# Performance work log

Measured on AMD Instinct MI355X. Metric: run time of the kernel, lower is better.

## Reference

```python
import jax, jax.numpy as jnp
import numpy as np

D_IN = 1024
D_OUT = 1024


def setup_inputs() -> dict:
    key = jax.random.key(0)
    kx, kq, kk, kv = jax.random.split(key, 4)
    x = jax.random.normal(kx, (4, 2048, D_IN), dtype=jnp.float32)
    s = 1.0 / np.sqrt(D_IN)
    Wq = jax.random.normal(kq, (D_IN, D_OUT), dtype=jnp.float32) * s
    Wk = jax.random.normal(kk, (D_IN, D_OUT), dtype=jnp.float32) * s
    Wv = jax.random.normal(kv, (D_IN, D_OUT), dtype=jnp.float32) * s
    return {"x": x, "Wq": Wq, "Wk": Wk, "Wv": Wv}


def reference(x, Wq, Wk, Wv):
    # x: [B, S, d_in]; W*: [d_in, d_out]
    B, S, _ = x.shape
    q = x @ Wq  # [B, S, d_out]
    k = x @ Wk
    v = x @ Wv
    scale = 1.0 / jnp.sqrt(jnp.asarray(k.shape[-1], x.dtype))
    scores = jnp.einsum("bqd,bkd->bqk", q, k) * scale  # [B, S, S]
    # causal mask: positions j > i masked to -inf (triu, diagonal=1)
    causal = jnp.tril(jnp.ones((S, S), dtype=bool))
    scores = jnp.where(causal[None, :, :], scores, -jnp.inf)
    attn = jax.nn.softmax(scores, axis=-1)  # dropout p=0.0 -> identity
    return jnp.einsum("bqk,bkd->bqd", attn, v)
```

## Files before the change

kernel.cpp:

```cpp
#include <hip/hip_runtime.h>
#include <hip/hip_bf16.h>

#define NB 4
#define SB 2048
#define DD 1024
#define BM 128
#define BN 128
#define BK 32

typedef __attribute__((ext_vector_type(8))) short bf16x8;
typedef __attribute__((ext_vector_type(4))) short bf16x4;
typedef __attribute__((ext_vector_type(4))) float f32x4;
typedef unsigned int u32;

__device__ __forceinline__ float bf2f(unsigned short u) {
    return __uint_as_float(((u32)u) << 16);
}
__device__ __forceinline__ short f2bf(float f) {
    u32 u = __float_as_uint(f);
    u32 r = (u + 0x7fffu + ((u >> 16) & 1u)) >> 16;
    return (short)r;
}

__device__ __forceinline__ void mfma_step(const short* As, const short* Bs,
                                          f32x4 (&acc)[4][4], int lane, int wave)
{
    const int wm = (wave >> 1) * 64, wn = (wave & 1) * 64;
    const int fr = lane & 15;
    const int quad = lane >> 4;
    bf16x8 af[4], bf[4];
#pragma unroll
    for (int t = 0; t < 4; t++) {
        af[t] = *(const bf16x8*)&As[(wm + t * 16 + fr) * BK + quad * 8];
        bf[t] = *(const bf16x8*)&Bs[(wn + t * 16 + fr) * BK + quad * 8];
    }
#pragma unroll
    for (int mt = 0; mt < 4; mt++)
#pragma unroll
        for (int nt = 0; nt < 4; nt++)
            acc[mt][nt] = __builtin_amdgcn_mfma_f32_16x16x32_bf16(
                af[mt], bf[nt], acc[mt][nt], 0, 0, 0);
}

__device__ __forceinline__ void stage128x32(const short* __restrict__ g, int ld,
                                            short* lds, int tid) {
    const int wave = tid >> 6, lane = tid & 63;
    const int r = lane >> 2;
    const int c = (lane & 3) * 8;
#pragma unroll
    for (int i = 0; i < 2; i++) {
        const int chunk = wave * 2 + i;
        const short* gp = g + (size_t)(chunk * 16 + r) * ld + c;
        __builtin_amdgcn_global_load_lds(
            (const __attribute__((address_space(1))) u32*)gp,
            (__attribute__((address_space(3))) u32*)(lds + chunk * 512 + lane * 8),
            16, 0, 0);
    }
}

__device__ __forceinline__ void stage_f32_128x32(const float* __restrict__ g,
                                                 int ld, short* lds, int tid) {
    const int r = tid >> 1;
    const int c = (tid & 1) * 16;
    const float* gp = &g[(size_t)r * ld + c];
    float4 v0 = *(const float4*)(gp + 0);
    float4 v1 = *(const float4*)(gp + 4);
    float4 v2 = *(const float4*)(gp + 8);
    float4 v3 = *(const float4*)(gp + 12);
    bf16x8 o0, o1;
    o0[0] = f2bf(v0.x); o0[1] = f2bf(v0.y); o0[2] = f2bf(v0.z); o0[3] = f2bf(v0.w);
    o0[4] = f2bf(v1.x); o0[5] = f2bf(v1.y); o0[6] = f2bf(v1.z); o0[7] = f2bf(v1.w);
    o1[0] = f2bf(v2.x); o1[1] = f2bf(v2.y); o1[2] = f2bf(v2.z); o1[3] = f2bf(v2.w);
    o1[4] = f2bf(v3.x); o1[5] = f2bf(v3.y); o1[6] = f2bf(v3.z); o1[7] = f2bf(v3.w);
    *(bf16x8*)&lds[r * BK + c] = o0;
    *(bf16x8*)&lds[r * BK + c + 8] = o1;
}

__device__ __forceinline__ void gemm_bt_body(
    const short* __restrict__ A, int lda, const short* __restrict__ Bt, int ldb,
    int m0, int n0, int kend, short* As, short* Bs, f32x4 (&acc)[4][4], int tid)
{
    const int lane = tid & 63;
    const int wave = tid >> 6;
    for (int k0 = 0; k0 < kend; k0 += BK) {
        stage128x32(A + (size_t)m0 * lda + k0, lda, As, tid);
        stage128x32(Bt + (size_t)n0 * ldb + k0, ldb, Bs, tid);
        __syncthreads();
        mfma_step(As, Bs, acc, lane, wave);
        __syncthreads();
    }
}

__global__ __launch_bounds__(256) void prep_mm(
    const float* __restrict__ x, const float* __restrict__ Wq,
    const float* __restrict__ Wk, const float* __restrict__ Wv,
    short* __restrict__ xb, short* __restrict__ Wvt, float* __restrict__ Mp4)
{
    __shared__ short As[BM * BK], Bs[BN * BK];
    __shared__ short t[64][65];
    const int bx = blockIdx.x;
    const int tid = threadIdx.x;
    if (bx < 256) {
        const int ch = bx >> 6;
        const int t64 = bx & 63;
        const int m0 = (t64 >> 3) * BM;
        const int n0 = (t64 & 7) * BN;
        const int kbase = ch * 256;
        const int lane = tid & 63, wave = tid >> 6;
        f32x4 acc[4][4];
#pragma unroll
        for (int a = 0; a < 4; a++)
#pragma unroll
            for (int b = 0; b < 4; b++) acc[a][b] = (f32x4){0.f, 0.f, 0.f, 0.f};
        for (int k0 = 0; k0 < 256; k0 += BK) {
            stage_f32_128x32(Wk + (size_t)m0 * DD + kbase + k0, DD, As, tid);
            stage_f32_128x32(Wq + (size_t)n0 * DD + kbase + k0, DD, Bs, tid);
            __syncthreads();
            mfma_step(As, Bs, acc, lane, wave);
            __syncthreads();
        }
        const int wm = (wave >> 1) * 64, wn = (wave & 1) * 64;
        const int fr = lane & 15, quad = lane >> 4;
        float* Mc = Mp4 + (size_t)ch * DD * DD;
#pragma unroll
        for (int mt = 0; mt < 4; mt++)
#pragma unroll
            for (int nt = 0; nt < 4; nt++)
#pragma unroll
                for (int r = 0; r < 4; r++) {
                    const size_t m = m0 + wm + mt * 16 + quad * 4 + r;
                    const size_t n = n0 + wn + nt * 16 + fr;
                    Mc[m * DD + n] = acc[mt][nt][r];
                }
        return;
    }
    if (bx < 4352) {
        const size_t i = ((size_t)(bx - 256) * 256 + tid) * 8;
        float4 a = *(const float4*)&x[i];
        float4 b = *(const float4*)&x[i + 4];
        bf16x8 o;
        o[0] = f2bf(a.x); o[1] = f2bf(a.y); o[2] = f2bf(a.z); o[3] = f2bf(a.w);
        o[4] = f2bf(b.x); o[5] = f2bf(b.y); o[6] = f2bf(b.z); o[7] = f2bf(b.w);
        *(bf16x8*)&xb[i] = o;
        return;
    }
    const int rr = bx - 4352;
    const int k0 = (rr & 15) * 64;
    const int n0 = (rr >> 4) * 64;
    {
        const int r = tid >> 4;
        const int c = (tid & 15) * 4;
#pragma unroll
        for (int i = 0; i < 4; i++) {
            float4 v = *(const float4*)&Wv[(size_t)(k0 + i * 16 + r) * DD + n0 + c];
            t[i * 16 + r][c + 0] = f2bf(v.x);
            t[i * 16 + r][c + 1] = f2bf(v.y);
            t[i * 16 + r][c + 2] = f2bf(v.z);
            t[i * 16 + r][c + 3] = f2bf(v.w);
        }
    }
    __syncthreads();
    {
        const int r = tid >> 3;
        const int c = (tid & 7) * 8;
#pragma unroll
        for (int i = 0; i < 2; i++) {
            bf16x8 o;
#pragma unroll
            for (int j = 0; j < 8; j++) o[j] = t[c + j][i * 32 + r];
            *(bf16x8*)&Wvt[(size_t)(n0 + i * 32 + r) * DD + k0 + c] = o;
        }
    }
}

__global__ __launch_bounds__(256) void mm_reduce(const float* __restrict__ Mp4,
                                                 short* __restrict__ Mp)
{
    const size_t e = ((size_t)blockIdx.x * 256 + threadIdx.x) * 4;
    const size_t N = (size_t)DD * DD;
    float4 s = *(const float4*)&Mp4[e];
#pragma unroll
    for (int c = 1; c < 4; c++) {
        float4 p = *(const float4*)&Mp4[c * N + e];
        s.x += p.x; s.y += p.y; s.z += p.z; s.w += p.w;
    }
    bf16x4 o;
    o[0] = f2bf(s.x); o[1] = f2bf(s.y); o[2] = f2bf(s.z); o[3] = f2bf(s.w);
    *(bf16x4*)&Mp[e] = o;
}

__global__ __launch_bounds__(256) void t_gemm(
    const short* __restrict__ xb, const short* __restrict__ Mp,
    short* __restrict__ T)
{
    __shared__ short As[BM * BK], Bs[BN * BK];
    const int n0 = blockIdx.x * BN;
    const int m0 = blockIdx.y * BM;
    f32x4 acc[4][4];
#pragma unroll
    for (int a = 0; a < 4; a++)
#pragma unroll
        for (int b = 0; b < 4; b++) acc[a][b] = (f32x4){0.f, 0.f, 0.f, 0.f};
    gemm_bt_body(xb, DD, Mp, DD, m0, n0, DD, As, Bs, acc, threadIdx.x);
    const int lane = threadIdx.x & 63, wave = threadIdx.x >> 6;
    const int wm = (wave >> 1) * 64, wn = (wave & 1) * 64;
    const int fr = lane & 15, quad = lane >> 4;
#pragma unroll
    for (int mt = 0; mt < 4; mt++)
#pragma unroll
        for (int nt = 0; nt < 4; nt++)
#pragma unroll
            for (int r = 0; r < 4; r++) {
                const size_t m = m0 + wm + mt * 16 + quad * 4 + r;
                const size_t n = n0 + wn + nt * 16 + fr;
                T[m * DD + n] = f2bf(acc[mt][nt][r]);
            }
}

__global__ __launch_bounds__(256) void v_gemm(
    const short* __restrict__ xb, const short* __restrict__ Wvt,
    short* __restrict__ Vt)
{
    __shared__ short As[BM * BK], Bs[BN * BK];
    const int n0 = blockIdx.x * BN;
    const int m0 = blockIdx.y * BM;
    f32x4 acc[4][4];
#pragma unroll
    for (int a = 0; a < 4; a++)
#pragma unroll
        for (int b = 0; b < 4; b++) acc[a][b] = (f32x4){0.f, 0.f, 0.f, 0.f};
    gemm_bt_body(xb, DD, Wvt, DD, m0, n0, DD, As, Bs, acc, threadIdx.x);
    const int lane = threadIdx.x & 63, wave = threadIdx.x >> 6;
    const int wm = (wave >> 1) * 64, wn = (wave & 1) * 64;
    const int fr = lane & 15, quad = lane >> 4;
    const int bb = m0 >> 11;
    const int s0 = (m0 & (SB - 1)) + wm + quad * 4;
    short* Vb = Vt + (size_t)bb * DD * SB;
#pragma unroll
    for (int mt = 0; mt < 4; mt++)
#pragma unroll
        for (int nt = 0; nt < 4; nt++) {
            const size_t n = n0 + wn + nt * 16 + fr;
            const size_t s = s0 + mt * 16;
            bf16x4 o;
#pragma unroll
            for (int r = 0; r < 4; r++) o[r] = f2bf(acc[mt][nt][r]);
            *(bf16x4*)&Vb[n * SB + s] = o;
        }
}

__global__ __launch_bounds__(256) void scores_mfma(
    const short* __restrict__ T, const short* __restrict__ xb,
    short* __restrict__ Sc)
{
    const int idx = blockIdx.x;
    int qt = (int)((__fsqrt_rn(8.f * idx + 1.f) - 1.f) * 0.5f);
    while ((qt + 1) * (qt + 2) / 2 <= idx) qt++;
    while (qt * (qt + 1) / 2 > idx) qt--;
    const int kt = idx - qt * (qt + 1) / 2;
    const int qm0 = qt * BM;
    const int kn0 = kt * BN;
    const int b = blockIdx.y;
    __shared__ short As[BM * BK], Bs[BN * BK];
    const short* Tb = T + (size_t)b * SB * DD;
    const short* Xb = xb + (size_t)b * SB * DD;
    short* Sb = Sc + (size_t)b * SB * SB;
    f32x4 acc[4][4];
#pragma unroll
    for (int a = 0; a < 4; a++)
#pragma unroll
        for (int c = 0; c < 4; c++) acc[a][c] = (f32x4){0.f, 0.f, 0.f, 0.f};
    gemm_bt_body(Tb, DD, Xb, DD, qm0, kn0, DD, As, Bs, acc, threadIdx.x);
    const int lane = threadIdx.x & 63, wave = threadIdx.x >> 6;
    const int wm = (wave >> 1) * 64, wn = (wave & 1) * 64;
    const int fr = lane & 15, quad = lane >> 4;
    const float scale = 0.03125f;
#pragma unroll
    for (int mt = 0; mt < 4; mt++)
#pragma unroll
        for (int nt = 0; nt < 4; nt++)
#pragma unroll
            for (int r = 0; r < 4; r++) {
                const size_t q = qm0 + wm + mt * 16 + quad * 4 + r;
                const size_t k = kn0 + wn + nt * 16 + fr;
                Sb[q * SB + k] = f2bf(acc[mt][nt][r] * scale);
            }
}

__global__ __launch_bounds__(256) void softmax_kernel(short* __restrict__ Sc)
{
    const int row = blockIdx.x;
    const int i = row & (SB - 1);
    const int jlim = ((i >> 7) + 1) << 7;
    short* r = Sc + (size_t)row * SB;
    const int t = threadIdx.x;
    const int lane = t & 63, wave = t >> 6;
    __shared__ float red[8];

    float v[8];
    float mx = -1e30f;
#pragma unroll
    for (int c = 0; c < 8; c++) {
        const int j = c * 256 + t;
        const float s = (j <= i) ? bf2f((unsigned short)r[j]) : -1e30f;
        v[c] = s;
        mx = fmaxf(mx, s);
    }
#pragma unroll
    for (int o = 32; o > 0; o >>= 1) mx = fmaxf(mx, __shfl_down(mx, o));
    if (lane == 0) red[wave] = mx;
    __syncthreads();
    mx = fmaxf(fmaxf(red[0], red[1]), fmaxf(red[2], red[3]));

    float sum = 0.f;
#pragma unroll
    for (int c = 0; c < 8; c++) {
        const int j = c * 256 + t;
        const float e = (j <= i) ? __expf(v[c] - mx) : 0.f;
        v[c] = e;
        sum += e;
    }
#pragma unroll
    for (int o = 32; o > 0; o >>= 1) sum += __shfl_down(sum, o);
    if (lane == 0) red[4 + wave] = sum;
    __syncthreads();
    const float inv = 1.0f / (red[4] + red[5] + red[6] + red[7]);
#pragma unroll
    for (int c = 0; c < 8; c++) {
        const int j = c * 256 + t;
        if (j < jlim) r[j] = f2bf(v[c] * inv);
    }
}

__global__ __launch_bounds__(256) void pv_mfma(
    const short* __restrict__ P, const short* __restrict__ Vt,
    float* __restrict__ O, float* __restrict__ Pp)
{
    __shared__ short As[BM * BK], Bs[BN * BK];
    const int n0 = blockIdx.x * BN;
    const int y = blockIdx.y;
    const int chunk1 = (y >= 16);
    const int qt = chunk1 ? (y - 8) : y;
    const int qm0 = qt * BM;
    const int kstart = chunk1 ? 1024 : 0;
    const int kstop = chunk1 ? (qt + 1) * BM : min(1024, (qt + 1) * BM);
    const int b = blockIdx.z;
    const short* Pb = P + (size_t)b * SB * SB + kstart;
    const short* Vb = Vt + (size_t)b * DD * SB + kstart;
    f32x4 acc[4][4];
#pragma unroll
    for (int a = 0; a < 4; a++)
#pragma unroll
        for (int c = 0; c < 4; c++) acc[a][c] = (f32x4){0.f, 0.f, 0.f, 0.f};
    gemm_bt_body(Pb, SB, Vb, SB, qm0, n0, kstop - kstart, As, Bs, acc,
                 threadIdx.x);
    const int lane = threadIdx.x & 63, wave = threadIdx.x >> 6;
    const int wm = (wave >> 1) * 64, wn = (wave & 1) * 64;
    const int fr = lane & 15, quad = lane >> 4;
    float* dst = chunk1 ? (Pp + (size_t)b * 1024 * DD)
                        : (O + (size_t)b * SB * DD);
    const int qoff = chunk1 ? 1024 : 0;
#pragma unroll
    for (int mt = 0; mt < 4; mt++)
#pragma unroll
        for (int nt = 0; nt < 4; nt++)
#pragma unroll
            for (int r = 0; r < 4; r++) {
                const size_t q = qm0 + wm + mt * 16 + quad * 4 + r - qoff;
                const size_t n = n0 + wn + nt * 16 + fr;
                dst[q * DD + n] = acc[mt][nt][r];
            }
}

__global__ __launch_bounds__(256) void reduce_pv(const float* __restrict__ Pp,
                                                 float* __restrict__ O)
{
    const size_t e = ((size_t)blockIdx.x * 256 + threadIdx.x) * 4;
    const size_t b = e / ((size_t)1024 * DD);
    const size_t rem = e - b * (size_t)1024 * DD;
    float4 p = *(const float4*)&Pp[e];
    float* o = &O[b * (size_t)SB * DD + (size_t)1024 * DD + rem];
    float4 v = *(const float4*)o;
    v.x += p.x; v.y += p.y; v.z += p.z; v.w += p.w;
    *(float4*)o = v;
}

extern "C" void kernel_launch(void* const* d_in, const int* in_sizes, int n_in,
                              void* d_out, int out_size, void* d_ws, size_t ws_size,
                              hipStream_t stream)
{
    const float* x  = (const float*)d_in[0];
    const float* Wq = (const float*)d_in[1];
    const float* Wk = (const float*)d_in[2];
    const float* Wv = (const float*)d_in[3];
    float* out = (float*)d_out;

    const size_t XE = (size_t)NB * SB * DD;
    const size_t WE = (size_t)DD * DD;
    short* xb  = (short*)d_ws;
    short* T   = xb + XE;
    short* Vt  = T + XE;
    short* Sc  = Vt + XE;
    float* Pp  = (float*)(Sc + (size_t)NB * SB * SB);
    short* Wvt = (short*)(Pp + (size_t)NB * 1024 * DD);
    short* Mp  = Wvt + WE;
    float* Mp4 = (float*)Sc;

    prep_mm<<<dim3(256 + 4096 + 256), 256, 0, stream>>>(
        x, Wq, Wk, Wv, xb, Wvt, Mp4);
    mm_reduce<<<dim3(1024), 256, 0, stream>>>(Mp4, Mp);
    t_gemm<<<dim3(DD / BN, (NB * SB) / BM), 256, 0, stream>>>(xb, Mp, T);
    v_gemm<<<dim3(DD / BN, (NB * SB) / BM), 256, 0, stream>>>(xb, Wvt, Vt);
    scores_mfma<<<dim3(136, NB), 256, 0, stream>>>(T, xb, Sc);
    softmax_kernel<<<dim3(NB * SB), 256, 0, stream>>>(Sc);
    pv_mfma<<<dim3(DD / BN, 24, NB), 256, 0, stream>>>(Sc, Vt, out, Pp);
    reduce_pv<<<dim3((unsigned)((size_t)NB * 1024 * DD / 4 / 256)), 256, 0,
                stream>>>(Pp, out);
}
```

Measured before the change: 266.3 us.

## Double-buffer GEMM LDS staging, merge T/V GEMMs, pair PV tiles, vectorize softmax

The shared GEMM loop now uses two LDS buffers, so the next K-slice is staged while the MFMAs run on the current one, with one barrier per iteration instead of two. The T and V projection GEMMs become a single launch using a z-dimension selector. The PV kernel no longer splits K into partial sums that need a separate reduce kernel; each block handles a complementary pair of causal query tiles to balance work. Softmax now loads and stores eight contiguous bf16 values per thread instead of strided scalars. LDS per block doubles, and the larger PV blocks give fewer blocks for occupancy.

```diff
diff --git a/kernel.cpp b/kernel.cpp
--- a/kernel.cpp
+++ b/kernel.cpp
@@ -76,17 +76,26 @@
     *(bf16x8*)&lds[r * BK + c + 8] = o1;
 }
 
-__device__ __forceinline__ void gemm_bt_body(
+__device__ __forceinline__ void gemm_bt_body_db(
     const short* __restrict__ A, int lda, const short* __restrict__ Bt, int ldb,
-    int m0, int n0, int kend, short* As, short* Bs, f32x4 (&acc)[4][4], int tid)
+    int kend, short* As, short* Bs, f32x4 (&acc)[4][4], int tid)
 {
     const int lane = tid & 63;
     const int wave = tid >> 6;
+    stage128x32(A, lda, As, tid);
+    stage128x32(Bt, ldb, Bs, tid);
+    __syncthreads();
     for (int k0 = 0; k0 < kend; k0 += BK) {
-        stage128x32(A + (size_t)m0 * lda + k0, lda, As, tid);
-        stage128x32(Bt + (size_t)n0 * ldb + k0, ldb, Bs, tid);
-        __syncthreads();
-        mfma_step(As, Bs, acc, lane, wave);
+        const int cur = (k0 >> 5) & 1;
+        const short* as = As + cur * (BM * BK);
+        const short* bs = Bs + cur * (BN * BK);
+        if (k0 + BK < kend) {
+            short* an = As + (cur ^ 1) * (BM * BK);
+            short* bn = Bs + (cur ^ 1) * (BN * BK);
+            stage128x32(A + k0 + BK, lda, an, tid);
+            stage128x32(Bt + k0 + BK, ldb, bn, tid);
+        }
+        mfma_step(as, bs, acc, lane, wave);
         __syncthreads();
     }
 }
@@ -189,64 +198,53 @@
     *(bf16x4*)&Mp[e] = o;
 }
 
-__global__ __launch_bounds__(256) void t_gemm(
+__global__ __launch_bounds__(256) void tv_gemm(
     const short* __restrict__ xb, const short* __restrict__ Mp,
-    short* __restrict__ T)
-{
-    __shared__ short As[BM * BK], Bs[BN * BK];
+    const short* __restrict__ Wvt, short* __restrict__ T,
+    short* __restrict__ Vt)
+{
+    __shared__ short As[2 * BM * BK], Bs[2 * BN * BK];
     const int n0 = blockIdx.x * BN;
     const int m0 = blockIdx.y * BM;
+    const int isv = blockIdx.z;
+    const short* Bt = isv ? Wvt : Mp;
     f32x4 acc[4][4];
 #pragma unroll
     for (int a = 0; a < 4; a++)
 #pragma unroll
         for (int b = 0; b < 4; b++) acc[a][b] = (f32x4){0.f, 0.f, 0.f, 0.f};
-    gemm_bt_body(xb, DD, Mp, DD, m0, n0, DD, As, Bs, acc, threadIdx.x);
+    gemm_bt_body_db(xb + (size_t)m0 * DD, DD, Bt + (size_t)n0 * DD, DD, DD,
+                    As, Bs, acc, threadIdx.x);
     const int lane = threadIdx.x & 63, wave = threadIdx.x >> 6;
     const int wm = (wave >> 1) * 64, wn = (wave & 1) * 64;
     const int fr = lane & 15, quad = lane >> 4;
-#pragma unroll
-    for (int mt = 0; mt < 4; mt++)
-#pragma unroll
-        for (int nt = 0; nt < 4; nt++)
-#pragma unroll
-            for (int r = 0; r < 4; r++) {
-                const size_t m = m0 + wm + mt * 16 + quad * 4 + r;
+    if (!isv) {
+#pragma unroll
+        for (int mt = 0; mt < 4; mt++)
+#pragma unroll
+            for (int nt = 0; nt < 4; nt++)
+#pragma unroll
+                for (int r = 0; r < 4; r++) {
+                    const size_t m = m0 + wm + mt * 16 + quad * 4 + r;
+                    const size_t n = n0 + wn + nt * 16 + fr;
+                    T[m * DD + n] = f2bf(acc[mt][nt][r]);
+                }
+    } else {
+        const int bb = m0 >> 11;
+        const int s0 = (m0 & (SB - 1)) + wm + quad * 4;
+        short* Vb = Vt + (size_t)bb * DD * SB;
+#pragma unroll
+        for (int mt = 0; mt < 4; mt++)
+#pragma unroll
+            for (int nt = 0; nt < 4; nt++) {
                 const size_t n = n0 + wn + nt * 16 + fr;
-                T[m * DD + n] = f2bf(acc[mt][nt][r]);
+                const size_t s = s0 + mt * 16;
+                bf16x4 o;
+#pragma unroll
+                for (int r = 0; r < 4; r++) o[r] = f2bf(acc[mt][nt][r]);
+                *(bf16x4*)&Vb[n * SB + s] = o;
             }
-}
-
-__global__ __launch_bounds__(256) void v_gemm(
-    const short* __restrict__ xb, const short* __restrict__ Wvt,
-    short* __restrict__ Vt)
-{
-    __shared__ short As[BM * BK], Bs[BN * BK];
-    const int n0 = blockIdx.x * BN;
-    const int m0 = blockIdx.y * BM;
-    f32x4 acc[4][4];
-#pragma unroll
-    for (int a = 0; a < 4; a++)
-#pragma unroll
-        for (int b = 0; b < 4; b++) acc[a][b] = (f32x4){0.f, 0.f, 0.f, 0.f};
-    gemm_bt_body(xb, DD, Wvt, DD, m0, n0, DD, As, Bs, acc, threadIdx.x);
-    const int lane = threadIdx.x & 63, wave = threadIdx.x >> 6;
-    const int wm = (wave >> 1) * 64, wn = (wave & 1) * 64;
-    const int fr = lane & 15, quad = lane >> 4;
-    const int bb = m0 >> 11;
-    const int s0 = (m0 & (SB - 1)) + wm + quad * 4;
-    short* Vb = Vt + (size_t)bb * DD * SB;
-#pragma unroll
-    for (int mt = 0; mt < 4; mt++)
-#pragma unroll
-        for (int nt = 0; nt < 4; nt++) {
-            const size_t n = n0 + wn + nt * 16 + fr;
-            const size_t s = s0 + mt * 16;
-            bf16x4 o;
-#pragma unroll
-            for (int r = 0; r < 4; r++) o[r] = f2bf(acc[mt][nt][r]);
-            *(bf16x4*)&Vb[n * SB + s] = o;
-        }
+    }
 }
 
 __global__ __launch_bounds__(256) void scores_mfma(
@@ -261,7 +259,7 @@
     const int qm0 = qt * BM;
     const int kn0 = kt * BN;
     const int b = blockIdx.y;
-    __shared__ short As[BM * BK], Bs[BN * BK];
+    __shared__ short As[2 * BM * BK], Bs[2 * BN * BK];
     const short* Tb = T + (size_t)b * SB * DD;
     const short* Xb = xb + (size_t)b * SB * DD;
     short* Sb = Sc + (size_t)b * SB * SB;
@@ -270,7 +268,8 @@
     for (int a = 0; a < 4; a++)
 #pragma unroll
         for (int c = 0; c < 4; c++) acc[a][c] = (f32x4){0.f, 0.f, 0.f, 0.f};
-    gemm_bt_body(Tb, DD, Xb, DD, qm0, kn0, DD, As, Bs, acc, threadIdx.x);
+    gemm_bt_body_db(Tb + (size_t)qm0 * DD, DD, Xb + (size_t)kn0 * DD, DD, DD,
+                    As, Bs, acc, threadIdx.x);
     const int lane = threadIdx.x & 63, wave = threadIdx.x >> 6;
     const int wm = (wave >> 1) * 64, wn = (wave & 1) * 64;
     const int fr = lane & 15, quad = lane >> 4;
@@ -297,13 +296,14 @@
     const int lane = t & 63, wave = t >> 6;
     __shared__ float red[8];
 
+    const int j0 = t * 8;
+    bf16x8 in = *(const bf16x8*)&r[j0];
     float v[8];
     float mx = -1e30f;
 #pragma unroll
-    for (int c = 0; c < 8; c++) {
-        const int j = c * 256 + t;
-        const float s = (j <= i) ? bf2f((unsigned short)r[j]) : -1e30f;
-        v[c] = s;
+    for (int e = 0; e < 8; e++) {
+        const float s = (j0 + e <= i) ? bf2f((unsigned short)in[e]) : -1e30f;
+        v[e] = s;
         mx = fmaxf(mx, s);
     }
 #pragma unroll
@@ -314,75 +314,60 @@
 
     float sum = 0.f;
 #pragma unroll
-    for (int c = 0; c < 8; c++) {
-        const int j = c * 256 + t;
-        const float e = (j <= i) ? __expf(v[c] - mx) : 0.f;
-        v[c] = e;
-        sum += e;
+    for (int e = 0; e < 8; e++) {
+        const float x = (j0 + e <= i) ? __expf(v[e] - mx) : 0.f;
+        v[e] = x;
+        sum += x;
     }
 #pragma unroll
     for (int o = 32; o > 0; o >>= 1) sum += __shfl_down(sum, o);
     if (lane == 0) red[4 + wave] = sum;
     __syncthreads();
     const float inv = 1.0f / (red[4] + red[5] + red[6] + red[7]);
-#pragma unroll
-    for (int c = 0; c < 8; c++) {
-        const int j = c * 256 + t;
-        if (j < jlim) r[j] = f2bf(v[c] * inv);
+    if (j0 < jlim) {
+        bf16x8 o;
+#pragma unroll
+        for (int e = 0; e < 8; e++) o[e] = f2bf(v[e] * inv);
+        *(bf16x8*)&r[j0] = o;
     }
 }
 
 __global__ __launch_bounds__(256) void pv_mfma(
     const short* __restrict__ P, const short* __restrict__ Vt,
-    float* __restrict__ O, float* __restrict__ Pp)
-{
-    __shared__ short As[BM * BK], Bs[BN * BK];
+    float* __restrict__ O)
+{
+    __shared__ short As[2 * BM * BK], Bs[2 * BN * BK];
     const int n0 = blockIdx.x * BN;
-    const int y = blockIdx.y;
-    const int chunk1 = (y >= 16);
-    const int qt = chunk1 ? (y - 8) : y;
-    const int qm0 = qt * BM;
-    const int kstart = chunk1 ? 1024 : 0;
-    const int kstop = chunk1 ? (qt + 1) * BM : min(1024, (qt + 1) * BM);
+    const int pair = blockIdx.y;
     const int b = blockIdx.z;
-    const short* Pb = P + (size_t)b * SB * SB + kstart;
-    const short* Vb = Vt + (size_t)b * DD * SB + kstart;
-    f32x4 acc[4][4];
-#pragma unroll
-    for (int a = 0; a < 4; a++)
-#pragma unroll
-        for (int c = 0; c < 4; c++) acc[a][c] = (f32x4){0.f, 0.f, 0.f, 0.f};
-    gemm_bt_body(Pb, SB, Vb, SB, qm0, n0, kstop - kstart, As, Bs, acc,
-                 threadIdx.x);
+    const short* Pb = P + (size_t)b * SB * SB;
+    const short* Vb = Vt + (size_t)b * DD * SB;
+    float* Ob = O + (size_t)b * SB * DD;
     const int lane = threadIdx.x & 63, wave = threadIdx.x >> 6;
     const int wm = (wave >> 1) * 64, wn = (wave & 1) * 64;
     const int fr = lane & 15, quad = lane >> 4;
-    float* dst = chunk1 ? (Pp + (size_t)b * 1024 * DD)
-                        : (O + (size_t)b * SB * DD);
-    const int qoff = chunk1 ? 1024 : 0;
-#pragma unroll
-    for (int mt = 0; mt < 4; mt++)
-#pragma unroll
-        for (int nt = 0; nt < 4; nt++)
-#pragma unroll
-            for (int r = 0; r < 4; r++) {
-                const size_t q = qm0 + wm + mt * 16 + quad * 4 + r - qoff;
-                const size_t n = n0 + wn + nt * 16 + fr;
-                dst[q * DD + n] = acc[mt][nt][r];
-            }
-}
-
-__global__ __launch_bounds__(256) void reduce_pv(const float* __restrict__ Pp,
-                                                 float* __restrict__ O)
-{
-    const size_t e = ((size_t)blockIdx.x * 256 + threadIdx.x) * 4;
-    const size_t b = e / ((size_t)1024 * DD);
-    const size_t rem = e - b * (size_t)1024 * DD;
-    float4 p = *(const float4*)&Pp[e];
-    float* o = &O[b * (size_t)SB * DD + (size_t)1024 * DD + rem];
-    float4 v = *(const float4*)o;
-    v.x += p.x; v.y += p.y; v.z += p.z; v.w += p.w;
-    *(float4*)o = v;
+    for (int half = 0; half < 2; ++half) {
+        const int qt = half ? (15 - pair) : pair;
+        const int qm0 = qt * BM;
+        const int kend = (qt + 1) * BM;
+        f32x4 acc[4][4];
+#pragma unroll
+        for (int a = 0; a < 4; a++)
+#pragma unroll
+            for (int c = 0; c < 4; c++) acc[a][c] = (f32x4){0.f, 0.f, 0.f, 0.f};
+        gemm_bt_body_db(Pb + (size_t)qm0 * SB, SB, Vb + (size_t)n0 * SB, SB,
+                        kend, As, Bs, acc, threadIdx.x);
+#pragma unroll
+        for (int mt = 0; mt < 4; mt++)
+#pragma unroll
+            for (int nt = 0; nt < 4; nt++)
+#pragma unroll
+                for (int r = 0; r < 4; r++) {
+                    const size_t q = qm0 + wm + mt * 16 + quad * 4 + r;
+                    const size_t n = n0 + wn + nt * 16 + fr;
+                    Ob[q * DD + n] = acc[mt][nt][r];
+                }
+    }
 }
 
 extern "C" void kernel_launch(void* const* d_in, const int* in_sizes, int n_in,
@@ -409,11 +394,9 @@
     prep_mm<<<dim3(256 + 4096 + 256), 256, 0, stream>>>(
         x, Wq, Wk, Wv, xb, Wvt, Mp4);
     mm_reduce<<<dim3(1024), 256, 0, stream>>>(Mp4, Mp);
-    t_gemm<<<dim3(DD / BN, (NB * SB) / BM), 256, 0, stream>>>(xb, Mp, T);
-    v_gemm<<<dim3(DD / BN, (NB * SB) / BM), 256, 0, stream>>>(xb, Wvt, Vt);
+    tv_gemm<<<dim3(DD / BN, (NB * SB) / BM, 2), 256, 0, stream>>>(
+        xb, Mp, Wvt, T, Vt);
     scores_mfma<<<dim3(136, NB), 256, 0, stream>>>(T, xb, Sc);
     softmax_kernel<<<dim3(NB * SB), 256, 0, stream>>>(Sc);
-    pv_mfma<<<dim3(DD / BN, 24, NB), 256, 0, stream>>>(Sc, Vt, out, Pp);
-    reduce_pv<<<dim3((unsigned)((size_t)NB * 1024 * DD / 4 / 256)), 256, 0,
-                stream>>>(Pp, out);
-}
+    pv_mfma<<<dim3(DD / BN, 8, NB), 256, 0, stream>>>(Sc, Vt, out);
+}
```

Measured after the change: 302.6 us. 13.6% more time.
